# Kernel tuning notes

Measured on AMD Instinct MI355X. Metric: run time of the kernel, lower is better.

Reference implementation:

```python
import jax, jax.numpy as jnp
import numpy as np

G = 64        # graphs per batch
NPG = 1024    # nodes per graph (static)
DEG = 8       # avg degree
INF = 128
HID = 256
OUT = 256
N = G * NPG
E = N * DEG
K1 = 512      # ceil(0.5 * 1024)
K2 = 256      # ceil(0.5 * 512)
EPS = 1e-5


def setup_inputs() -> dict:
    key = jax.random.key(0)
    ks = jax.random.split(key, 12)
    s = 0.05
    x = jax.random.normal(ks[0], (N, INF), jnp.float32)
    off = (jnp.arange(G, dtype=jnp.int32) * NPG)[:, None]
    src = (jax.random.randint(ks[1], (G, NPG * DEG), 0, NPG, jnp.int32) + off).reshape(-1)
    dst = (jax.random.randint(ks[2], (G, NPG * DEG), 0, NPG, jnp.int32) + off).reshape(-1)
    return {
        'x': x, 'src': src, 'dst': dst,
        'W_rel1': jax.random.normal(ks[3], (INF, HID), jnp.float32) * s,
        'b_rel1': jnp.zeros((HID,), jnp.float32),
        'W_root1': jax.random.normal(ks[4], (INF, HID), jnp.float32) * s,
        'g1': jnp.ones((HID,), jnp.float32), 'bt1': jnp.zeros((HID,), jnp.float32),
        'p1': jax.random.normal(ks[5], (HID,), jnp.float32) * s,
        'g2': jnp.ones((HID,), jnp.float32), 'bt2': jnp.zeros((HID,), jnp.float32),
        'W_rel2': jax.random.normal(ks[6], (HID, HID), jnp.float32) * s,
        'b_rel2': jnp.zeros((HID,), jnp.float32),
        'W_root2': jax.random.normal(ks[7], (HID, HID), jnp.float32) * s,
        'p2': jax.random.normal(ks[8], (HID,), jnp.float32) * s,
        'Wl': jax.random.normal(ks[9], (2 * HID, OUT), jnp.float32) * s,
        'bl': jnp.zeros((OUT,), jnp.float32),
    }


def _bn(x, g, b):
    # training-mode BatchNorm over nodes (biased variance), as nn.BatchNorm1d
    m = x.mean(0)
    v = x.var(0)
    return (x - m) * jax.lax.rsqrt(v + EPS) * g + b


def _conv(x, src, dst, emask, W_rel, b_rel, W_root):
    # GraphConv: sum_{j->i} x_j, then lin_rel(aggr) + lin_root(x)
    msg = x[src]                                    # [E, F] gather
    if emask is not None:
        msg = jnp.where(emask[:, None], msg, 0.0)   # dropped edges contribute 0
    agg = jax.ops.segment_sum(msg, dst, num_segments=x.shape[0])
    return agg @ W_rel + b_rel + x @ W_root


def _pool(x, src, dst, emask, p, n, k):
    # TopKPooling: score = tanh((x.p)/||p||); keep top-k per graph; x *= score
    score = jnp.tanh((x @ p) / jnp.linalg.norm(p))  # [G*n]
    vals, idx = jax.lax.top_k(score.reshape(G, n), k)   # [G, k] per-graph
    perm = (idx + (jnp.arange(G, dtype=jnp.int32) * n)[:, None]).reshape(-1)
    xn = x[perm] * vals.reshape(-1)[:, None]        # [G*k, F]
    # remap old node ids -> new ids; -1 marks dropped nodes
    mapping = jnp.full((G * n,), -1, jnp.int32).at[perm].set(
        jnp.arange(G * k, dtype=jnp.int32))
    ns, nd = mapping[src], mapping[dst]
    nmask = emask & (ns >= 0) & (nd >= 0)
    ns = jnp.where(nmask, ns, 0)
    nd = jnp.where(nmask, nd, 0)
    return xn, ns, nd, nmask


def reference(x, src, dst, W_rel1, b_rel1, W_root1, g1, bt1, p1,
              g2, bt2, W_rel2, b_rel2, W_root2, p2, Wl, bl):
    act = lambda v: jax.nn.gelu(v, approximate=False)
    h = _conv(x, src, dst, None, W_rel1, b_rel1, W_root1)
    h = _bn(act(h), g1, bt1)
    h, s1, d1, m1 = _pool(h, src, dst, jnp.ones((E,), bool), p1, NPG, K1)
    hg = h.reshape(G, K1, HID)
    x1 = jnp.concatenate([hg.max(1), hg.mean(1)], axis=1)   # [G, 2H] gmp|gap
    h = act(_bn(h, g2, bt2))
    h = _conv(h, s1, d1, m1, W_rel2, b_rel2, W_root2)
    h, s2, d2, m2 = _pool(h, s1, d1, m1, p2, K1, K2)
    hg = h.reshape(G, K2, HID)
    x2 = jnp.concatenate([hg.max(1), hg.mean(1)], axis=1)
    return (x1 + x2) @ Wl + bl                              # [G, OUT]
```

## Files before the change

### kernel.cpp

```cpp
#include <hip/hip_runtime.h>
#include <hip/hip_bf16.h>
#include <float.h>

#define GG    64
#define NPG   1024
#define EPG   8192
#define NE    524288
#define FIN   128
#define HID   256
#define K1    512
#define K2    256
#define NN0   65536
#define NN1   32768
#define NN2   16384
#define EPSBN 1e-5f

typedef _Float16 f16x8 __attribute__((ext_vector_type(8)));
typedef _Float16 f16x4 __attribute__((ext_vector_type(4)));
typedef float f32x4 __attribute__((ext_vector_type(4)));

__device__ __forceinline__ float gelu_exact(float v) {
    return 0.5f * v * (1.0f + erff(v * 0.7071067811865476f));
}

__device__ __forceinline__ void gld16(const void* g, void* lds) {
    __builtin_amdgcn_global_load_lds(
        (const __attribute__((address_space(1))) unsigned int*)g,
        (__attribute__((address_space(3))) unsigned int*)lds, 16, 0, 0);
}

__global__ __launch_bounds__(256) void k_prep(
        const float* __restrict__ Wrel1, const float* __restrict__ Wroot1,
        const float* __restrict__ Wrel2, const float* __restrict__ Wroot2,
        const float* __restrict__ p2,
        _Float16* __restrict__ W1h, _Float16* __restrict__ W1l,
        _Float16* __restrict__ W2h, _Float16* __restrict__ W2l,
        float* __restrict__ q2, float* __restrict__ stats1,
        float* __restrict__ stats2) {
    const int b = blockIdx.x, tid = threadIdx.x;
    if (b < 256) {
        const int i = b * 256 + tid;
        const int n = i >> 8, k = i & 255;
        const float v = (k < FIN) ? Wrel1[k * HID + n] : Wroot1[(k - FIN) * HID + n];
        const _Float16 hi = (_Float16)v;
        W1h[i] = hi;
        W1l[i] = (_Float16)((v - (float)hi) * 2048.0f);
    } else if (b < 768) {
        const int i = (b - 256) * 256 + tid;
        const int n = i >> 9, k = i & 511;
        const float v = (k < HID) ? Wrel2[k * HID + n] : Wroot2[(k - HID) * HID + n];
        const _Float16 hi = (_Float16)v;
        W2h[i] = hi;
        W2l[i] = (_Float16)((v - (float)hi) * 2048.0f);
    } else if (b == 768) {
        __shared__ float red[256];
        const float pv = p2[tid];
        red[tid] = pv * pv;
        __syncthreads();
        for (int s = 128; s > 0; s >>= 1) {
            if (tid < s) red[tid] += red[tid + s];
            __syncthreads();
        }
        q2[tid] = pv * rsqrtf(red[0]);
    } else {
        stats1[tid] = 0.f; stats1[256 + tid] = 0.f;
        stats2[tid] = 0.f; stats2[256 + tid] = 0.f;
    }
}

__global__ __launch_bounds__(512) void k_csr(const int* __restrict__ src,
        const int* __restrict__ dst, int* __restrict__ rowp,
        int* __restrict__ ssrc, int* __restrict__ map1) {
    __shared__ int cnt[NPG];
    __shared__ int sa[NPG];
    __shared__ int sb[NPG];
    const int g = blockIdx.x, tid = threadIdx.x;
    const int eb = g * EPG;
    for (int i = g * 512 + tid; i < NN0; i += GG * 512) map1[i] = -1;
    for (int i = tid; i < NPG; i += 512) cnt[i] = 0;
    __syncthreads();
    for (int e = tid; e < EPG; e += 512)
        atomicAdd(&cnt[dst[eb + e] & (NPG - 1)], 1);
    __syncthreads();
    for (int i = tid; i < NPG; i += 512) sa[i] = cnt[i];
    __syncthreads();
    int* cur = sa; int* nxt = sb;
    for (int d = 1; d < NPG; d <<= 1) {
        for (int i = tid; i < NPG; i += 512)
            nxt[i] = cur[i] + ((i >= d) ? cur[i - d] : 0);
        __syncthreads();
        int* t = cur; cur = nxt; nxt = t;
    }
    for (int i = tid; i < NPG; i += 512) {
        const int st = cur[i] - cnt[i];
        rowp[g * (NPG + 1) + i] = st;
        cnt[i] = st;
    }
    if (tid == 0) rowp[g * (NPG + 1) + NPG] = EPG;
    __syncthreads();
    for (int e = tid; e < EPG; e += 512) {
        const int d = dst[eb + e] & (NPG - 1);
        const int p = atomicAdd(&cnt[d], 1);
        ssrc[eb + p] = src[eb + e] & (NPG - 1);
    }
}

__global__ __launch_bounds__(256) void k_agg1(const float* __restrict__ x,
        const int* __restrict__ rowp, const int* __restrict__ ssrc,
        _Float16* __restrict__ A1) {
    const int b = blockIdx.x;
    const int g = b & 63;
    const int ng = b >> 6;
    const int tid = threadIdx.x;
    const int ln = tid & 31;
    const int node = (ng << 3) + (tid >> 5);
    const int s0 = rowp[g * (NPG + 1) + node];
    const int s1 = rowp[g * (NPG + 1) + node + 1];
    const float4* x4 = reinterpret_cast<const float4*>(x);
    const size_t gb = (size_t)(g << 10) * 32;
    const int* sp = ssrc + (size_t)g * EPG;
    float4 acc = make_float4(0.f, 0.f, 0.f, 0.f);
    for (int j = s0; j < s1; ++j) {
        const float4 v = x4[gb + (size_t)sp[j] * 32 + ln];
        acc.x += v.x; acc.y += v.y; acc.z += v.z; acc.w += v.w;
    }
    const size_t rb = ((size_t)((g << 10) + node)) * 256;
    *reinterpret_cast<f16x4*>(&A1[rb + (ln << 2)]) =
        (f16x4){(_Float16)acc.x, (_Float16)acc.y, (_Float16)acc.z, (_Float16)acc.w};
    const float4 xv = x4[gb + (size_t)node * 32 + ln];
    *reinterpret_cast<f16x4*>(&A1[rb + 128 + (ln << 2)]) =
        (f16x4){(_Float16)xv.x, (_Float16)xv.y, (_Float16)xv.z, (_Float16)xv.w};
}

__global__ __launch_bounds__(256) void k_agg2(const _Float16* __restrict__ A2r,
        const int* __restrict__ rowp, const int* __restrict__ ssrc,
        const int* __restrict__ perm1, const int* __restrict__ map1,
        _Float16* __restrict__ A2w) {
    const int b = blockIdx.x;
    const int g = b & 63;
    const int ng = b >> 6;
    const int tid = threadIdx.x;
    const int ln = tid & 63;
    const int ni = (ng << 2) + (tid >> 6);
    const int on = perm1[(g << 9) + ni] & (NPG - 1);
    const int s0 = rowp[g * (NPG + 1) + on];
    const int s1 = rowp[g * (NPG + 1) + on + 1];
    const int* sp = ssrc + (size_t)g * EPG;
    const int* mp = map1 + ((size_t)g << 10);
    float4 acc = make_float4(0.f, 0.f, 0.f, 0.f);
    for (int j = s0; j < s1; ++j) {
        const int ms = mp[sp[j]];
        if (ms < 0) continue;
        const f16x4 v = *reinterpret_cast<const f16x4*>(
            &A2r[(size_t)ms * 512 + 256 + (ln << 2)]);
        acc.x += (float)v[0]; acc.y += (float)v[1];
        acc.z += (float)v[2]; acc.w += (float)v[3];
    }
    *reinterpret_cast<f16x4*>(&A2w[((size_t)((g << 9) + ni)) * 512 + (ln << 2)]) =
        (f16x4){(_Float16)acc.x, (_Float16)acc.y, (_Float16)acc.z, (_Float16)acc.w};
}

template<int K, int EPI>
__global__ __launch_bounds__(512, 4) void k_gemm3(
        const _Float16* __restrict__ A,
        const _Float16* __restrict__ Bh, const _Float16* __restrict__ Bl,
        const float* __restrict__ bias, _Float16* __restrict__ C,
        float* __restrict__ stats, const float* __restrict__ qv2,
        float* __restrict__ scores, int M) {
    __shared__ _Float16 Ash[3][128 * 32];
    __shared__ _Float16 Bsh[3][128 * 32];
    __shared__ _Float16 Bsl[3][128 * 32];
    __shared__ float csum[128];
    __shared__ float csq[128];
    const int tid = threadIdx.x;
    const int l = tid & 63, w = tid >> 6;
    const int wm = w >> 2, wn = w & 3;
    const int m0 = blockIdx.x * 128, n0 = blockIdx.y * 128;
    const int r16 = l & 15, kg = l >> 4;

    const int srow = (w << 4) + (l >> 2);
    const int swz = ((l & 3) ^ ((srow >> 1) & 3)) << 3;
    const size_t aoff = (size_t)(m0 + srow) * K + swz;
    const size_t boff = (size_t)(n0 + srow) * K + swz;
    const int ldsb = w << 10;

    f32x4 accH[4][2] = {};
    f32x4 accL[4][2] = {};

    constexpr int NI = K / 32;
    gld16(A + aoff, (char*)Ash[0] + ldsb);
    gld16(Bh + boff, (char*)Bsh[0] + ldsb);
    gld16(Bl + boff, (char*)Bsl[0] + ldsb);
    gld16(A + aoff + 32, (char*)Ash[1] + ldsb);
    gld16(Bh + boff + 32, (char*)Bsh[1] + ldsb);
    gld16(Bl + boff + 32, (char*)Bsl[1] + ldsb);

#pragma unroll
    for (int i = 0; i < NI; ++i) {
        const int k0 = i * 32;
        const int cur = i % 3;
        __builtin_amdgcn_s_barrier();
        if (i + 2 < NI) {
            const int nxt = (i + 2) % 3;
            gld16(A + aoff + k0 + 64, (char*)Ash[nxt] + ldsb);
            gld16(Bh + boff + k0 + 64, (char*)Bsh[nxt] + ldsb);
            gld16(Bl + boff + k0 + 64, (char*)Bsl[nxt] + ldsb);
            asm volatile("s_waitcnt vmcnt(6)" ::: "memory");
        } else if (i + 1 < NI) {
            asm volatile("s_waitcnt vmcnt(3)" ::: "memory");
        } else {
            asm volatile("s_waitcnt vmcnt(0)" ::: "memory");
        }
        __builtin_amdgcn_s_barrier();
        __builtin_amdgcn_sched_barrier(0);
        const char* ab = (const char*)Ash[cur];
        const char* bbh = (const char*)Bsh[cur];
        const char* bbl = (const char*)Bsl[cur];
        f16x8 af[4], bfh[2], bfl[2];
#pragma unroll
        for (int mi = 0; mi < 4; ++mi) {
            const int r = wm * 64 + mi * 16 + r16;
            const int bo = r * 64 + ((kg ^ ((r >> 1) & 3)) << 4);
            af[mi] = *reinterpret_cast<const f16x8*>(ab + bo);
        }
#pragma unroll
        for (int ni = 0; ni < 2; ++ni) {
            const int r = wn * 32 + ni * 16 + r16;
            const int bo = r * 64 + ((kg ^ ((r >> 1) & 3)) << 4);
            bfh[ni] = *reinterpret_cast<const f16x8*>(bbh + bo);
            bfl[ni] = *reinterpret_cast<const f16x8*>(bbl + bo);
        }
#pragma unroll
        for (int mi = 0; mi < 4; ++mi)
#pragma unroll
            for (int ni = 0; ni < 2; ++ni) {
                accH[mi][ni] = __builtin_amdgcn_mfma_f32_16x16x32_f16(
                    af[mi], bfh[ni], accH[mi][ni], 0, 0, 0);
                accL[mi][ni] = __builtin_amdgcn_mfma_f32_16x16x32_f16(
                    af[mi], bfl[ni], accL[mi][ni], 0, 0, 0);
            }
    }

    if (EPI == 1) {
        if (tid < 128) { csum[tid] = 0.f; csq[tid] = 0.f; }
        __syncthreads();
    }

    float qv[2];
    if (EPI == 2) {
#pragma unroll
        for (int ni = 0; ni < 2; ++ni) qv[ni] = qv2[n0 + wn * 32 + ni * 16 + r16];
    }
    float sA[2] = {0, 0};
    float qA[2] = {0, 0};
    float sp[4][4] = {};
#pragma unroll
    for (int mi = 0; mi < 4; ++mi)
#pragma unroll
        for (int ni = 0; ni < 2; ++ni) {
            const int col = n0 + wn * 32 + ni * 16 + r16;
            const float bc = bias[col];
#pragma unroll
            for (int r = 0; r < 4; ++r) {
                const int row = m0 + wm * 64 + mi * 16 + (kg << 2) + r;
                float t = accH[mi][ni][r] + accL[mi][ni][r] * (1.0f / 2048.0f) + bc;
                if (EPI == 1) {
                    t = gelu_exact(t);
                    sA[ni] += t;
                    qA[ni] += t * t;
                }
                if (EPI == 2) sp[mi][r] += t * qv[ni];
                C[(size_t)row * 256 + col] = (_Float16)t;
            }
        }
    if (EPI == 1) {
#pragma unroll
        for (int ni = 0; ni < 2; ++ni) {
            const int cl = wn * 32 + ni * 16 + r16;
            unsafeAtomicAdd(&csum[cl], sA[ni]);
            unsafeAtomicAdd(&csq[cl], qA[ni]);
        }
        __syncthreads();
        if (tid < 128) {
            unsafeAtomicAdd(&stats[n0 + tid], csum[tid]);
            unsafeAtomicAdd(&stats[HID + n0 + tid], csq[tid]);
        }
    }
    if (EPI == 2) {
        const int slot = (int)blockIdx.y * 4 + wn;
#pragma unroll
        for (int mi = 0; mi < 4; ++mi)
#pragma unroll
            for (int r = 0; r < 4; ++r) {
                float s = sp[mi][r];
                s += __shfl_xor(s, 1);
                s += __shfl_xor(s, 2);
                s += __shfl_xor(s, 4);
                s += __shfl_xor(s, 8);
                if (r16 == 0)
                    scores[(size_t)slot * M + m0 + wm * 64 + mi * 16 + (kg << 2) + r] = s;
            }
    }
}

__global__ __launch_bounds__(256) void k_finalize1(const float* __restrict__ stats,
        const float* __restrict__ g1, const float* __restrict__ bt1,
        const float* __restrict__ p1, float* __restrict__ scale,
        float* __restrict__ shift, float* __restrict__ q, float* __restrict__ r) {
    __shared__ float red[256];
    const int c = threadIdx.x;
    const float m = stats[c] * (1.f / NN0);
    const float v = stats[HID + c] * (1.f / NN0) - m * m;
    const float sc = g1[c] * rsqrtf(v + EPSBN);
    const float sh = bt1[c] - m * sc;
    scale[c] = sc;
    shift[c] = sh;
    const float pv = p1[c];
    red[c] = pv * pv;
    __syncthreads();
    for (int s = 128; s > 0; s >>= 1) {
        if (c < s) red[c] += red[c + s];
        __syncthreads();
    }
    const float inv = rsqrtf(red[0]);
    q[c] = sc * pv * inv;
    __syncthreads();
    red[c] = sh * pv * inv;
    __syncthreads();
    for (int s = 128; s > 0; s >>= 1) {
        if (c < s) red[c] += red[c + s];
        __syncthreads();
    }
    if (c == 0) r[0] = red[0];
}

__global__ __launch_bounds__(256) void k_finalize2(const float* __restrict__ stats,
        const float* __restrict__ g2, const float* __restrict__ bt2,
        float* __restrict__ scale, float* __restrict__ shift) {
    const int c = threadIdx.x;
    const float m = stats[c] * (1.f / NN1);
    const float v = stats[HID + c] * (1.f / NN1) - m * m;
    const float sc = g2[c] * rsqrtf(v + EPSBN);
    scale[c] = sc;
    shift[c] = bt2[c] - m * sc;
}

__global__ __launch_bounds__(256) void k_score(const _Float16* __restrict__ H,
        const float* __restrict__ q, const float* __restrict__ r,
        float* __restrict__ out) {
    const int node = blockIdx.x * 4 + (threadIdx.x >> 6);
    const int lane = threadIdx.x & 63;
    const f16x4 h = *reinterpret_cast<const f16x4*>(H + (size_t)node * HID + (lane << 2));
    const float4 qv = *reinterpret_cast<const float4*>(q + (lane << 2));
    float d = (float)h[0] * qv.x + (float)h[1] * qv.y +
              (float)h[2] * qv.z + (float)h[3] * qv.w;
#pragma unroll
    for (int off = 32; off > 0; off >>= 1) d += __shfl_xor(d, off);
    if (lane == 0) out[node] = d + (r ? r[0] : 0.f);
}

template<int NN_, int KK_, int NT_>
__global__ __launch_bounds__(NT_) void k_topk(const float* __restrict__ scores,
        int nparts, int pstride, int* __restrict__ perm,
        float* __restrict__ vals, int* __restrict__ mapping) {
    __shared__ float s[NN_];
    __shared__ int id[NN_];
    const int g = blockIdx.x, tid = threadIdx.x;
    for (int i = tid; i < NN_; i += NT_) {
        float raw = 0.f;
        for (int p = 0; p < nparts; ++p)
            raw += scores[(size_t)p * pstride + g * NN_ + i];
        s[i] = tanhf(raw);
        id[i] = i;
    }
    __syncthreads();
    for (int k = 2; k <= NN_; k <<= 1) {
        for (int j = k >> 1; j > 0; j >>= 1) {
            for (int t = tid; t < NN_; t += NT_) {
                const int ixj = t ^ j;
                if (ixj > t) {
                    const bool desc = ((t & k) == 0);
                    const float s1 = s[t], s2 = s[ixj];
                    const int i1 = id[t], i2 = id[ixj];
                    const bool inOrder = (s1 > s2) || (s1 == s2 && i1 < i2);
                    if (inOrder != desc) { s[t] = s2; s[ixj] = s1; id[t] = i2; id[ixj] = i1; }
                }
            }
            __syncthreads();
        }
    }
    for (int i = tid; i < KK_; i += NT_) {
        const int oid = id[i];
        perm[g * KK_ + i] = g * NN_ + oid;
        vals[g * KK_ + i] = s[i];
        if (mapping) mapping[g * NN_ + oid] = g * KK_ + i;
    }
}

__global__ __launch_bounds__(256) void k_pool1p(const _Float16* __restrict__ HG,
        const int* __restrict__ perm, const float* __restrict__ vals,
        const float* __restrict__ scale1, const float* __restrict__ shift1,
        _Float16* __restrict__ H1P, float* __restrict__ pmax,
        float* __restrict__ psum, float* __restrict__ psq) {
    const int b = blockIdx.x;
    const int g = b >> 3, ig = b & 7;
    const int c = threadIdx.x;
    const float sc = scale1[c], sh = shift1[c];
    float mx = -FLT_MAX, sm = 0.f, sq = 0.f;
    for (int i = ig * 64; i < ig * 64 + 64; ++i) {
        const int idx = (g << 9) + i;
        const int srow = perm[idx];
        const float val = vals[idx];
        const float hv = (float)HG[(size_t)srow * HID + c];
        const float xn = (hv * sc + sh) * val;
        H1P[(size_t)idx * HID + c] = (_Float16)xn;
        mx = fmaxf(mx, xn);
        sm += xn;
        sq += xn * xn;
    }
    pmax[b * 256 + c] = mx;
    psum[b * 256 + c] = sm;
    psq[b * 256 + c] = sq;
}

__global__ __launch_bounds__(256) void k_pool1r(const float* __restrict__ pmax,
        const float* __restrict__ psum, const float* __restrict__ psq,
        float* __restrict__ X1, float* __restrict__ stats2) {
    const int g = blockIdx.x, c = threadIdx.x;
    float mx = -FLT_MAX, sm = 0.f, sq = 0.f;
    for (int ig = 0; ig < 8; ++ig) {
        const int o = ((g << 3) + ig) * 256 + c;
        mx = fmaxf(mx, pmax[o]);
        sm += psum[o];
        sq += psq[o];
    }
    X1[g * 512 + c] = mx;
    X1[g * 512 + 256 + c] = sm * (1.f / K1);
    unsafeAtomicAdd(&stats2[c], sm);
    unsafeAtomicAdd(&stats2[HID + c], sq);
}

__global__ __launch_bounds__(256) void k_h2in(const _Float16* __restrict__ H1P,
        const float* __restrict__ scale2, const float* __restrict__ shift2,
        _Float16* __restrict__ A2) {
    const int total = NN1 * (HID / 4);
    for (int i = blockIdx.x * 256 + threadIdx.x; i < total; i += gridDim.x * 256) {
        const int r = i >> 6, c4 = i & 63;
        const f16x4 v = reinterpret_cast<const f16x4*>(H1P)[i];
        const float4 sc = reinterpret_cast<const float4*>(scale2)[c4];
        const float4 sh = reinterpret_cast<const float4*>(shift2)[c4];
        *reinterpret_cast<f16x4*>(&A2[(size_t)r * 512 + 256 + (c4 << 2)]) =
            (f16x4){(_Float16)gelu_exact((float)v[0] * sc.x + sh.x),
                    (_Float16)gelu_exact((float)v[1] * sc.y + sh.y),
                    (_Float16)gelu_exact((float)v[2] * sc.z + sh.z),
                    (_Float16)gelu_exact((float)v[3] * sc.w + sh.w)};
    }
}

__global__ __launch_bounds__(256) void k_x2p(const _Float16* __restrict__ H2,
        const int* __restrict__ perm, const float* __restrict__ vals,
        float* __restrict__ pmax, float* __restrict__ psum) {
    const int b = blockIdx.x;
    const int g = b >> 3, ig = b & 7;
    const int c = threadIdx.x;
    float mx = -FLT_MAX, sm = 0.f;
    for (int i = ig * 32; i < ig * 32 + 32; ++i) {
        const int idx = (g << 8) + i;
        const int srow = perm[idx];
        const float v = (float)H2[(size_t)srow * HID + c] * vals[idx];
        mx = fmaxf(mx, v);
        sm += v;
    }
    pmax[b * 256 + c] = mx;
    psum[b * 256 + c] = sm;
}

__global__ __launch_bounds__(256) void k_x2r(const float* __restrict__ pmax,
        const float* __restrict__ psum, float* __restrict__ X2) {
    const int g = blockIdx.x, c = threadIdx.x;
    float mx = -FLT_MAX, sm = 0.f;
    for (int ig = 0; ig < 8; ++ig) {
        const int o = ((g << 3) + ig) * 256 + c;
        mx = fmaxf(mx, pmax[o]);
        sm += psum[o];
    }
    X2[g * 512 + c] = mx;
    X2[g * 512 + 256 + c] = sm * (1.f / K2);
}

__global__ __launch_bounds__(256) void k_final(const float* __restrict__ X1,
        const float* __restrict__ X2, const float* __restrict__ Wl,
        const float* __restrict__ bl, float* __restrict__ out) {
    const int g = blockIdx.x, c = threadIdx.x;
    float acc = bl[c];
    for (int k = 0; k < 512; ++k) {
        const float xv = X1[g * 512 + k] + X2[g * 512 + k];
        acc = fmaf(xv, Wl[k * HID + c], acc);
    }
    out[g * HID + c] = acc;
}

extern "C" void kernel_launch(void* const* d_in, const int* in_sizes, int n_in,
                              void* d_out, int out_size, void* d_ws, size_t ws_size,
                              hipStream_t stream) {
    (void)in_sizes; (void)n_in; (void)out_size; (void)ws_size;
    const float* x       = (const float*)d_in[0];
    const int*   src     = (const int*)  d_in[1];
    const int*   dst     = (const int*)  d_in[2];
    const float* W_rel1  = (const float*)d_in[3];
    const float* b_rel1  = (const float*)d_in[4];
    const float* W_root1 = (const float*)d_in[5];
    const float* g1      = (const float*)d_in[6];
    const float* bt1     = (const float*)d_in[7];
    const float* p1      = (const float*)d_in[8];
    const float* g2      = (const float*)d_in[9];
    const float* bt2     = (const float*)d_in[10];
    const float* W_rel2  = (const float*)d_in[11];
    const float* b_rel2  = (const float*)d_in[12];
    const float* W_root2 = (const float*)d_in[13];
    const float* p2      = (const float*)d_in[14];
    const float* Wl      = (const float*)d_in[15];
    const float* bl      = (const float*)d_in[16];
    float* out = (float*)d_out;

    char* w = (char*)d_ws;
    size_t off = 0;
    auto alloc = [&](size_t bytes) -> void* {
        void* p = w + off;
        off += (bytes + 255) & ~(size_t)255;
        return p;
    };
    _Float16* A1  = (_Float16*)alloc((size_t)NN0 * 256 * 2);
    _Float16* HG  = (_Float16*)alloc((size_t)NN0 * 256 * 2);
    _Float16* H2  = (_Float16*)alloc((size_t)NN1 * 256 * 2);
    int*   ROWP   = (int*)  alloc((size_t)GG * (NPG + 1) * 4);
    int*   SSRC   = (int*)  alloc((size_t)NE * 4);
    float* SCORES = (float*)alloc((size_t)8 * NN1 * 4);
    int*   PERM1  = (int*)  alloc((size_t)NN1 * 4);
    float* VALS1  = (float*)alloc((size_t)NN1 * 4);
    int*   MAP1   = (int*)  alloc((size_t)NN0 * 4);
    int*   PERM2  = (int*)  alloc((size_t)NN2 * 4);
    float* VALS2  = (float*)alloc((size_t)NN2 * 4);
    float* STATS1 = (float*)alloc(512 * 4);
    float* STATS2 = (float*)alloc(512 * 4);
    float* SCALE1 = (float*)alloc(256 * 4);
    float* SHIFT1 = (float*)alloc(256 * 4);
    float* Q1     = (float*)alloc(256 * 4);
    float* R1     = (float*)alloc(256);
    float* SCALE2 = (float*)alloc(256 * 4);
    float* SHIFT2 = (float*)alloc(256 * 4);
    float* Q2     = (float*)alloc(256 * 4);
    _Float16* W1h = (_Float16*)alloc((size_t)256 * 256 * 2);
    _Float16* W1l = (_Float16*)alloc((size_t)256 * 256 * 2);
    _Float16* W2h = (_Float16*)alloc((size_t)256 * 512 * 2);
    _Float16* W2l = (_Float16*)alloc((size_t)256 * 512 * 2);
    float* X1     = (float*)alloc((size_t)GG * 512 * 4);
    float* X2     = (float*)alloc((size_t)GG * 512 * 4);
    float* PMAX   = (float*)alloc((size_t)512 * 256 * 4);
    float* PSUM   = (float*)alloc((size_t)512 * 256 * 4);
    float* PSQ    = (float*)alloc((size_t)512 * 256 * 4);
    _Float16* H1P = A1;
    _Float16* A2 = HG;

    k_prep<<<770, 256, 0, stream>>>(W_rel1, W_root1, W_rel2, W_root2, p2,
        W1h, W1l, W2h, W2l, Q2, STATS1, STATS2);
    k_csr<<<GG, 512, 0, stream>>>(src, dst, ROWP, SSRC, MAP1);
    k_agg1<<<8192, 256, 0, stream>>>(x, ROWP, SSRC, A1);
    k_gemm3<256, 1><<<dim3(512, 2), 512, 0, stream>>>(A1, W1h, W1l,
        b_rel1, HG, STATS1, nullptr, nullptr, NN0);
    k_finalize1<<<1, 256, 0, stream>>>(STATS1, g1, bt1, p1, SCALE1, SHIFT1, Q1, R1);
    k_score<<<NN0 / 4, 256, 0, stream>>>(HG, Q1, R1, SCORES);
    k_topk<NPG, K1, 512><<<GG, 512, 0, stream>>>(SCORES, 1, 0, PERM1, VALS1, MAP1);
    k_pool1p<<<512, 256, 0, stream>>>(HG, PERM1, VALS1, SCALE1, SHIFT1, H1P, PMAX, PSUM, PSQ);
    k_pool1r<<<GG, 256, 0, stream>>>(PMAX, PSUM, PSQ, X1, STATS2);
    k_finalize2<<<1, 256, 0, stream>>>(STATS2, g2, bt2, SCALE2, SHIFT2);
    k_h2in<<<2048, 256, 0, stream>>>(H1P, SCALE2, SHIFT2, A2);
    k_agg2<<<8192, 256, 0, stream>>>(A2, ROWP, SSRC, PERM1, MAP1, A2);
    k_gemm3<512, 2><<<dim3(256, 2), 512, 0, stream>>>(A2, W2h, W2l,
        b_rel2, H2, nullptr, Q2, SCORES, NN1);
    k_topk<K1, K2, 256><<<GG, 256, 0, stream>>>(SCORES, 8, NN1, PERM2, VALS2, nullptr);
    k_x2p<<<512, 256, 0, stream>>>(H2, PERM2, VALS2, PMAX, PSUM);
    k_x2r<<<GG, 256, 0, stream>>>(PMAX, PSUM, X2);
    k_final<<<GG, 256, 0, stream>>>(X1, X2, Wl, bl, out);
}
```

Before: 279.5 us.

## Drop split-fp16 weight correction, widen GEMM N-tile, fuse prep/csr and pooling kernels

```diff
diff --git a/kernel.cpp b/kernel.cpp
--- a/kernel.cpp
+++ b/kernel.cpp
@@ -29,79 +29,71 @@
         (__attribute__((address_space(3))) unsigned int*)lds, 16, 0, 0);
 }
 
-__global__ __launch_bounds__(256) void k_prep(
+__global__ __launch_bounds__(512) void k_prepcsr(
+        const int* __restrict__ src, const int* __restrict__ dst,
+        int* __restrict__ rowp, int* __restrict__ ssrc, int* __restrict__ map1,
         const float* __restrict__ Wrel1, const float* __restrict__ Wroot1,
         const float* __restrict__ Wrel2, const float* __restrict__ Wroot2,
         const float* __restrict__ p2,
-        _Float16* __restrict__ W1h, _Float16* __restrict__ W1l,
-        _Float16* __restrict__ W2h, _Float16* __restrict__ W2l,
+        _Float16* __restrict__ W1h, _Float16* __restrict__ W2h,
         float* __restrict__ q2, float* __restrict__ stats1,
         float* __restrict__ stats2) {
+    __shared__ int cnt[NPG];
+    __shared__ int sa[NPG];
+    __shared__ int sb[NPG];
+    __shared__ float red[256];
     const int b = blockIdx.x, tid = threadIdx.x;
-    if (b < 256) {
-        const int i = b * 256 + tid;
+    if (b < 64) {
+        const int g = b;
+        const int eb = g * EPG;
+        for (int i = g * 512 + tid; i < NN0; i += GG * 512) map1[i] = -1;
+        for (int i = tid; i < NPG; i += 512) cnt[i] = 0;
+        __syncthreads();
+        for (int e = tid; e < EPG; e += 512)
+            atomicAdd(&cnt[dst[eb + e] & (NPG - 1)], 1);
+        __syncthreads();
+        for (int i = tid; i < NPG; i += 512) sa[i] = cnt[i];
+        __syncthreads();
+        int* cur = sa; int* nxt = sb;
+        for (int d = 1; d < NPG; d <<= 1) {
+            for (int i = tid; i < NPG; i += 512)
+                nxt[i] = cur[i] + ((i >= d) ? cur[i - d] : 0);
+            __syncthreads();
+            int* t = cur; cur = nxt; nxt = t;
+        }
+        for (int i = tid; i < NPG; i += 512) {
+            const int st = cur[i] - cnt[i];
+            rowp[g * (NPG + 1) + i] = st;
+            cnt[i] = st;
+        }
+        if (tid == 0) rowp[g * (NPG + 1) + NPG] = EPG;
+        __syncthreads();
+        for (int e = tid; e < EPG; e += 512) {
+            const int d = dst[eb + e] & (NPG - 1);
+            const int p = atomicAdd(&cnt[d], 1);
+            ssrc[eb + p] = src[eb + e] & (NPG - 1);
+        }
+    } else if (b < 192) {
+        const int i = (b - 64) * 512 + tid;
         const int n = i >> 8, k = i & 255;
         const float v = (k < FIN) ? Wrel1[k * HID + n] : Wroot1[(k - FIN) * HID + n];
-        const _Float16 hi = (_Float16)v;
-        W1h[i] = hi;
-        W1l[i] = (_Float16)((v - (float)hi) * 2048.0f);
-    } else if (b < 768) {
-        const int i = (b - 256) * 256 + tid;
+        W1h[i] = (_Float16)v;
+    } else if (b < 448) {
+        const int i = (b - 192) * 512 + tid;
         const int n = i >> 9, k = i & 511;
         const float v = (k < HID) ? Wrel2[k * HID + n] : Wroot2[(k - HID) * HID + n];
-        const _Float16 hi = (_Float16)v;
-        W2h[i] = hi;
-        W2l[i] = (_Float16)((v - (float)hi) * 2048.0f);
-    } else if (b == 768) {
-        __shared__ float red[256];
-        const float pv = p2[tid];
-        red[tid] = pv * pv;
+        W2h[i] = (_Float16)v;
+    } else if (b == 448) {
+        if (tid < 256) { const float pv = p2[tid]; red[tid] = pv * pv; }
         __syncthreads();
         for (int s = 128; s > 0; s >>= 1) {
             if (tid < s) red[tid] += red[tid + s];
             __syncthreads();
         }
-        q2[tid] = pv * rsqrtf(red[0]);
+        if (tid < 256) q2[tid] = p2[tid] * rsqrtf(red[0]);
     } else {
-        stats1[tid] = 0.f; stats1[256 + tid] = 0.f;
-        stats2[tid] = 0.f; stats2[256 + tid] = 0.f;
-    }
-}
-
-__global__ __launch_bounds__(512) void k_csr(const int* __restrict__ src,
-        const int* __restrict__ dst, int* __restrict__ rowp,
-        int* __restrict__ ssrc, int* __restrict__ map1) {
-    __shared__ int cnt[NPG];
-    __shared__ int sa[NPG];
-    __shared__ int sb[NPG];
-    const int g = blockIdx.x, tid = threadIdx.x;
-    const int eb = g * EPG;
-    for (int i = g * 512 + tid; i < NN0; i += GG * 512) map1[i] = -1;
-    for (int i = tid; i < NPG; i += 512) cnt[i] = 0;
-    __syncthreads();
-    for (int e = tid; e < EPG; e += 512)
-        atomicAdd(&cnt[dst[eb + e] & (NPG - 1)], 1);
-    __syncthreads();
-    for (int i = tid; i < NPG; i += 512) sa[i] = cnt[i];
-    __syncthreads();
-    int* cur = sa; int* nxt = sb;
-    for (int d = 1; d < NPG; d <<= 1) {
-        for (int i = tid; i < NPG; i += 512)
-            nxt[i] = cur[i] + ((i >= d) ? cur[i - d] : 0);
-        __syncthreads();
-        int* t = cur; cur = nxt; nxt = t;
-    }
-    for (int i = tid; i < NPG; i += 512) {
-        const int st = cur[i] - cnt[i];
-        rowp[g * (NPG + 1) + i] = st;
-        cnt[i] = st;
-    }
-    if (tid == 0) rowp[g * (NPG + 1) + NPG] = EPG;
-    __syncthreads();
-    for (int e = tid; e < EPG; e += 512) {
-        const int d = dst[eb + e] & (NPG - 1);
-        const int p = atomicAdd(&cnt[d], 1);
-        ssrc[eb + p] = src[eb + e] & (NPG - 1);
+        stats1[tid] = 0.f;
+        stats2[tid] = 0.f;
     }
 }
 
@@ -161,39 +153,42 @@
 }
 
 template<int K, int EPI>
-__global__ __launch_bounds__(512, 4) void k_gemm3(
-        const _Float16* __restrict__ A,
-        const _Float16* __restrict__ Bh, const _Float16* __restrict__ Bl,
+__global__ __launch_bounds__(512, 4) void k_gemm(
+        const _Float16* __restrict__ A, const _Float16* __restrict__ B,
         const float* __restrict__ bias, _Float16* __restrict__ C,
         float* __restrict__ stats, const float* __restrict__ qv2,
         float* __restrict__ scores, int M) {
     __shared__ _Float16 Ash[3][128 * 32];
-    __shared__ _Float16 Bsh[3][128 * 32];
-    __shared__ _Float16 Bsl[3][128 * 32];
-    __shared__ float csum[128];
-    __shared__ float csq[128];
+    __shared__ _Float16 Bsh[3][256 * 32];
+    __shared__ float csum[256];
+    __shared__ float csq[256];
     const int tid = threadIdx.x;
     const int l = tid & 63, w = tid >> 6;
     const int wm = w >> 2, wn = w & 3;
-    const int m0 = blockIdx.x * 128, n0 = blockIdx.y * 128;
+    const int m0 = blockIdx.x * 128;
     const int r16 = l & 15, kg = l >> 4;
 
-    const int srow = (w << 4) + (l >> 2);
-    const int swz = ((l & 3) ^ ((srow >> 1) & 3)) << 3;
-    const size_t aoff = (size_t)(m0 + srow) * K + swz;
-    const size_t boff = (size_t)(n0 + srow) * K + swz;
-    const int ldsb = w << 10;
-
-    f32x4 accH[4][2] = {};
-    f32x4 accL[4][2] = {};
-
+    const int srA = (w << 4) + (l >> 2);
+    const int swA = ((l & 3) ^ ((srA >> 1) & 3)) << 3;
+    const size_t aoff = (size_t)(m0 + srA) * K + swA;
+    const int ldsA = w << 10;
+    const int srB0 = (w << 5) + (l >> 2);
+    const int srB1 = srB0 + 16;
+    const int swB0 = ((l & 3) ^ ((srB0 >> 1) & 3)) << 3;
+    const int swB1 = ((l & 3) ^ ((srB1 >> 1) & 3)) << 3;
+    const size_t boff0 = (size_t)srB0 * K + swB0;
+    const size_t boff1 = (size_t)srB1 * K + swB1;
+    const int ldsB0 = w << 11, ldsB1 = (w << 11) + 1024;
+
+    f32x4 acc[4][4] = {};
     constexpr int NI = K / 32;
-    gld16(A + aoff, (char*)Ash[0] + ldsb);
-    gld16(Bh + boff, (char*)Bsh[0] + ldsb);
-    gld16(Bl + boff, (char*)Bsl[0] + ldsb);
-    gld16(A + aoff + 32, (char*)Ash[1] + ldsb);
-    gld16(Bh + boff + 32, (char*)Bsh[1] + ldsb);
-    gld16(Bl + boff + 32, (char*)Bsl[1] + ldsb);
+
+    gld16(A + aoff,       (char*)Ash[0] + ldsA);
+    gld16(B + boff0,      (char*)Bsh[0] + ldsB0);
+    gld16(B + boff1,      (char*)Bsh[0] + ldsB1);
+    gld16(A + aoff + 32,  (char*)Ash[1] + ldsA);
+    gld16(B + boff0 + 32, (char*)Bsh[1] + ldsB0);
+    gld16(B + boff1 + 32, (char*)Bsh[1] + ldsB1);
 
 #pragma unroll
     for (int i = 0; i < NI; ++i) {
@@ -202,9 +197,9 @@
         __builtin_amdgcn_s_barrier();
         if (i + 2 < NI) {
             const int nxt = (i + 2) % 3;
-            gld16(A + aoff + k0 + 64, (char*)Ash[nxt] + ldsb);
-            gld16(Bh + boff + k0 + 64, (char*)Bsh[nxt] + ldsb);
-            gld16(Bl + boff + k0 + 64, (char*)Bsl[nxt] + ldsb);
+            gld16(A + aoff + k0 + 64,  (char*)Ash[nxt] + ldsA);
+            gld16(B + boff0 + k0 + 64, (char*)Bsh[nxt] + ldsB0);
+            gld16(B + boff1 + k0 + 64, (char*)Bsh[nxt] + ldsB1);
             asm volatile("s_waitcnt vmcnt(6)" ::: "memory");
         } else if (i + 1 < NI) {
             asm volatile("s_waitcnt vmcnt(3)" ::: "memory");
@@ -214,9 +209,8 @@
         __builtin_amdgcn_s_barrier();
         __builtin_amdgcn_sched_barrier(0);
         const char* ab = (const char*)Ash[cur];
-        const char* bbh = (const char*)Bsh[cur];
-        const char* bbl = (const char*)Bsl[cur];
-        f16x8 af[4], bfh[2], bfl[2];
+        const char* bb = (const char*)Bsh[cur];
+        f16x8 af[4], bf[4];
 #pragma unroll
         for (int mi = 0; mi < 4; ++mi) {
             const int r = wm * 64 + mi * 16 + r16;
@@ -224,46 +218,42 @@
             af[mi] = *reinterpret_cast<const f16x8*>(ab + bo);
         }
 #pragma unroll
-        for (int ni = 0; ni < 2; ++ni) {
-            const int r = wn * 32 + ni * 16 + r16;
+        for (int ni = 0; ni < 4; ++ni) {
+            const int r = wn * 64 + ni * 16 + r16;
             const int bo = r * 64 + ((kg ^ ((r >> 1) & 3)) << 4);
-            bfh[ni] = *reinterpret_cast<const f16x8*>(bbh + bo);
-            bfl[ni] = *reinterpret_cast<const f16x8*>(bbl + bo);
+            bf[ni] = *reinterpret_cast<const f16x8*>(bb + bo);
         }
 #pragma unroll
         for (int mi = 0; mi < 4; ++mi)
 #pragma unroll
-            for (int ni = 0; ni < 2; ++ni) {
-                accH[mi][ni] = __builtin_amdgcn_mfma_f32_16x16x32_f16(
-                    af[mi], bfh[ni], accH[mi][ni], 0, 0, 0);
-                accL[mi][ni] = __builtin_amdgcn_mfma_f32_16x16x32_f16(
-                    af[mi], bfl[ni], accL[mi][ni], 0, 0, 0);
-            }
+            for (int ni = 0; ni < 4; ++ni)
+                acc[mi][ni] = __builtin_amdgcn_mfma_f32_16x16x32_f16(
+                    af[mi], bf[ni], acc[mi][ni], 0, 0, 0);
     }
 
     if (EPI == 1) {
-        if (tid < 128) { csum[tid] = 0.f; csq[tid] = 0.f; }
-        __syncthreads();
-    }
-
-    float qv[2];
+        if (tid < 256) { csum[tid] = 0.f; csq[tid] = 0.f; }
+        __syncthreads();
+    }
+
+    float qv[4];
     if (EPI == 2) {
 #pragma unroll
-        for (int ni = 0; ni < 2; ++ni) qv[ni] = qv2[n0 + wn * 32 + ni * 16 + r16];
-    }
-    float sA[2] = {0, 0};
-    float qA[2] = {0, 0};
+        for (int ni = 0; ni < 4; ++ni) qv[ni] = qv2[wn * 64 + ni * 16 + r16];
+    }
+    float sA[4] = {0, 0, 0, 0};
+    float qA[4] = {0, 0, 0, 0};
     float sp[4][4] = {};
 #pragma unroll
     for (int mi = 0; mi < 4; ++mi)
 #pragma unroll
-        for (int ni = 0; ni < 2; ++ni) {
-            const int col = n0 + wn * 32 + ni * 16 + r16;
+        for (int ni = 0; ni < 4; ++ni) {
+            const int col = wn * 64 + ni * 16 + r16;
             const float bc = bias[col];
 #pragma unroll
             for (int r = 0; r < 4; ++r) {
                 const int row = m0 + wm * 64 + mi * 16 + (kg << 2) + r;
-                float t = accH[mi][ni][r] + accL[mi][ni][r] * (1.0f / 2048.0f) + bc;
+                float t = acc[mi][ni][r] + bc;
                 if (EPI == 1) {
                     t = gelu_exact(t);
                     sA[ni] += t;
@@ -275,19 +265,19 @@
         }
     if (EPI == 1) {
 #pragma unroll
-        for (int ni = 0; ni < 2; ++ni) {
-            const int cl = wn * 32 + ni * 16 + r16;
+        for (int ni = 0; ni < 4; ++ni) {
+            const int cl = wn * 64 + ni * 16 + r16;
             unsafeAtomicAdd(&csum[cl], sA[ni]);
             unsafeAtomicAdd(&csq[cl], qA[ni]);
         }
         __syncthreads();
-        if (tid < 128) {
-            unsafeAtomicAdd(&stats[n0 + tid], csum[tid]);
-            unsafeAtomicAdd(&stats[HID + n0 + tid], csq[tid]);
+        if (tid < 256) {
+            unsafeAtomicAdd(&stats[tid], csum[tid]);
+            unsafeAtomicAdd(&stats[HID + tid], csq[tid]);
         }
     }
     if (EPI == 2) {
-        const int slot = (int)blockIdx.y * 4 + wn;
+        const int slot = wn;
 #pragma unroll
         for (int mi = 0; mi < 4; ++mi)
 #pragma unroll
@@ -400,8 +390,8 @@
 __global__ __launch_bounds__(256) void k_pool1p(const _Float16* __restrict__ HG,
         const int* __restrict__ perm, const float* __restrict__ vals,
         const float* __restrict__ scale1, const float* __restrict__ shift1,
-        _Float16* __restrict__ H1P, float* __restrict__ pmax,
-        float* __restrict__ psum, float* __restrict__ psq) {
+        float* __restrict__ pmax, float* __restrict__ psum,
+        float* __restrict__ psq) {
     const int b = blockIdx.x;
     const int g = b >> 3, ig = b & 7;
     const int c = threadIdx.x;
@@ -413,7 +403,6 @@
         const float val = vals[idx];
         const float hv = (float)HG[(size_t)srow * HID + c];
         const float xn = (hv * sc + sh) * val;
-        H1P[(size_t)idx * HID + c] = (_Float16)xn;
         mx = fmaxf(mx, xn);
         sm += xn;
         sq += xn * xn;
@@ -440,21 +429,29 @@
     unsafeAtomicAdd(&stats2[HID + c], sq);
 }
 
-__global__ __launch_bounds__(256) void k_h2in(const _Float16* __restrict__ H1P,
+__global__ __launch_bounds__(256) void k_h2in(const _Float16* __restrict__ HG,
+        const int* __restrict__ perm, const float* __restrict__ vals,
+        const float* __restrict__ scale1, const float* __restrict__ shift1,
         const float* __restrict__ scale2, const float* __restrict__ shift2,
         _Float16* __restrict__ A2) {
-    const int total = NN1 * (HID / 4);
-    for (int i = blockIdx.x * 256 + threadIdx.x; i < total; i += gridDim.x * 256) {
-        const int r = i >> 6, c4 = i & 63;
-        const f16x4 v = reinterpret_cast<const f16x4*>(H1P)[i];
-        const float4 sc = reinterpret_cast<const float4*>(scale2)[c4];
-        const float4 sh = reinterpret_cast<const float4*>(shift2)[c4];
-        *reinterpret_cast<f16x4*>(&A2[(size_t)r * 512 + 256 + (c4 << 2)]) =
-            (f16x4){(_Float16)gelu_exact((float)v[0] * sc.x + sh.x),
-                    (_Float16)gelu_exact((float)v[1] * sc.y + sh.y),
-                    (_Float16)gelu_exact((float)v[2] * sc.z + sh.z),
-                    (_Float16)gelu_exact((float)v[3] * sc.w + sh.w)};
-    }
+    const int i = blockIdx.x * 256 + threadIdx.x;
+    const int idx = i >> 6, c4 = i & 63;
+    const int srow = perm[idx];
+    const float val = vals[idx];
+    const f16x4 h = *reinterpret_cast<const f16x4*>(&HG[(size_t)srow * HID + (c4 << 2)]);
+    const float4 s1 = reinterpret_cast<const float4*>(scale1)[c4];
+    const float4 b1 = reinterpret_cast<const float4*>(shift1)[c4];
+    const float4 s2 = reinterpret_cast<const float4*>(scale2)[c4];
+    const float4 b2 = reinterpret_cast<const float4*>(shift2)[c4];
+    const float x0 = ((float)h[0] * s1.x + b1.x) * val;
+    const float x1 = ((float)h[1] * s1.y + b1.y) * val;
+    const float x2 = ((float)h[2] * s1.z + b1.z) * val;
+    const float x3 = ((float)h[3] * s1.w + b1.w) * val;
+    *reinterpret_cast<f16x4*>(&A2[(size_t)idx * 512 + 256 + (c4 << 2)]) =
+        (f16x4){(_Float16)gelu_exact(x0 * s2.x + b2.x),
+                (_Float16)gelu_exact(x1 * s2.y + b2.y),
+                (_Float16)gelu_exact(x2 * s2.z + b2.z),
+                (_Float16)gelu_exact(x3 * s2.w + b2.w)};
 }
 
 __global__ __launch_bounds__(256) void k_x2p(const _Float16* __restrict__ H2,
@@ -475,8 +472,11 @@
     psum[b * 256 + c] = sm;
 }
 
-__global__ __launch_bounds__(256) void k_x2r(const float* __restrict__ pmax,
-        const float* __restrict__ psum, float* __restrict__ X2) {
+__global__ __launch_bounds__(256) void k_x2final(const float* __restrict__ pmax,
+        const float* __restrict__ psum, const float* __restrict__ X1,
+        const float* __restrict__ Wl, const float* __restrict__ bl,
+        float* __restrict__ out) {
+    __shared__ float sx2[512];
     const int g = blockIdx.x, c = threadIdx.x;
     float mx = -FLT_MAX, sm = 0.f;
     for (int ig = 0; ig < 8; ++ig) {
@@ -484,17 +484,12 @@
         mx = fmaxf(mx, pmax[o]);
         sm += psum[o];
     }
-    X2[g * 512 + c] = mx;
-    X2[g * 512 + 256 + c] = sm * (1.f / K2);
-}
-
-__global__ __launch_bounds__(256) void k_final(const float* __restrict__ X1,
-        const float* __restrict__ X2, const float* __restrict__ Wl,
-        const float* __restrict__ bl, float* __restrict__ out) {
-    const int g = blockIdx.x, c = threadIdx.x;
+    sx2[c] = mx;
+    sx2[256 + c] = sm * (1.f / K2);
+    __syncthreads();
     float acc = bl[c];
     for (int k = 0; k < 512; ++k) {
-        const float xv = X1[g * 512 + k] + X2[g * 512 + k];
+        const float xv = X1[g * 512 + k] + sx2[k];
         acc = fmaf(xv, Wl[k * HID + c], acc);
     }
     out[g * HID + c] = acc;
@@ -535,7 +530,7 @@
     _Float16* H2  = (_Float16*)alloc((size_t)NN1 * 256 * 2);
     int*   ROWP   = (int*)  alloc((size_t)GG * (NPG + 1) * 4);
     int*   SSRC   = (int*)  alloc((size_t)NE * 4);
-    float* SCORES = (float*)alloc((size_t)8 * NN1 * 4);
+    float* SCORES = (float*)alloc((size_t)4 * NN1 * 4);
     int*   PERM1  = (int*)  alloc((size_t)NN1 * 4);
     float* VALS1  = (float*)alloc((size_t)NN1 * 4);
     int*   MAP1   = (int*)  alloc((size_t)NN0 * 4);
@@ -551,35 +546,30 @@
     float* SHIFT2 = (float*)alloc(256 * 4);
     float* Q2     = (float*)alloc(256 * 4);
     _Float16* W1h = (_Float16*)alloc((size_t)256 * 256 * 2);
-    _Float16* W1l = (_Float16*)alloc((size_t)256 * 256 * 2);
     _Float16* W2h = (_Float16*)alloc((size_t)256 * 512 * 2);
-    _Float16* W2l = (_Float16*)alloc((size_t)256 * 512 * 2);
     float* X1     = (float*)alloc((size_t)GG * 512 * 4);
-    float* X2     = (float*)alloc((size_t)GG * 512 * 4);
     float* PMAX   = (float*)alloc((size_t)512 * 256 * 4);
     float* PSUM   = (float*)alloc((size_t)512 * 256 * 4);
     float* PSQ    = (float*)alloc((size_t)512 * 256 * 4);
-    _Float16* H1P = A1;
-    _Float16* A2 = HG;
-
-    k_prep<<<770, 256, 0, stream>>>(W_rel1, W_root1, W_rel2, W_root2, p2,
-        W1h, W1l, W2h, W2l, Q2, STATS1, STATS2);
-    k_csr<<<GG, 512, 0, stream>>>(src, dst, ROWP, SSRC, MAP1);
+    _Float16* A2 = A1;
+
+    k_prepcsr<<<450, 512, 0, stream>>>(src, dst, ROWP, SSRC, MAP1,
+        W_rel1, W_root1, W_rel2, W_root2, p2, W1h, W2h, Q2, STATS1, STATS2);
     k_agg1<<<8192, 256, 0, stream>>>(x, ROWP, SSRC, A1);
-    k_gemm3<256, 1><<<dim3(512, 2), 512, 0, stream>>>(A1, W1h, W1l,
-        b_rel1, HG, STATS1, nullptr, nullptr, NN0);
+    k_gemm<256, 1><<<512, 512, 0, stream>>>(A1, W1h, b_rel1, HG, STATS1,
+        nullptr, nullptr, NN0);
     k_finalize1<<<1, 256, 0, stream>>>(STATS1, g1, bt1, p1, SCALE1, SHIFT1, Q1, R1);
     k_score<<<NN0 / 4, 256, 0, stream>>>(HG, Q1, R1, SCORES);
     k_topk<NPG, K1, 512><<<GG, 512, 0, stream>>>(SCORES, 1, 0, PERM1, VALS1, MAP1);
-    k_pool1p<<<512, 256, 0, stream>>>(HG, PERM1, VALS1, SCALE1, SHIFT1, H1P, PMAX, PSUM, PSQ);
+    k_pool1p<<<512, 256, 0, stream>>>(HG, PERM1, VALS1, SCALE1, SHIFT1, PMAX, PSUM, PSQ);
     k_pool1r<<<GG, 256, 0, stream>>>(PMAX, PSUM, PSQ, X1, STATS2);
     k_finalize2<<<1, 256, 0, stream>>>(STATS2, g2, bt2, SCALE2, SHIFT2);
-    k_h2in<<<2048, 256, 0, stream>>>(H1P, SCALE2, SHIFT2, A2);
+    k_h2in<<<8192, 256, 0, stream>>>(HG, PERM1, VALS1, SCALE1, SHIFT1,
+        SCALE2, SHIFT2, A2);
     k_agg2<<<8192, 256, 0, stream>>>(A2, ROWP, SSRC, PERM1, MAP1, A2);
-    k_gemm3<512, 2><<<dim3(256, 2), 512, 0, stream>>>(A2, W2h, W2l,
-        b_rel2, H2, nullptr, Q2, SCORES, NN1);
-    k_topk<K1, K2, 256><<<GG, 256, 0, stream>>>(SCORES, 8, NN1, PERM2, VALS2, nullptr);
+    k_gemm<512, 2><<<256, 512, 0, stream>>>(A2, W2h, b_rel2, H2, nullptr,
+        Q2, SCORES, NN1);
+    k_topk<K1, K2, 256><<<GG, 256, 0, stream>>>(SCORES, 4, NN1, PERM2, VALS2, nullptr);
     k_x2p<<<512, 256, 0, stream>>>(H2, PERM2, VALS2, PMAX, PSUM);
-    k_x2r<<<GG, 256, 0, stream>>>(PMAX, PSUM, X2);
-    k_final<<<GG, 256, 0, stream>>>(X1, X2, Wl, bl, out);
-}
+    k_x2final<<<GG, 256, 0, stream>>>(PMAX, PSUM, X1, Wl, bl, out);
+}
```

Result: faster. 257.6 us (-7.8%).
